# Performance work log

Hardware: AMD Instinct MI355X
Metric: run time of the kernel (lower is better)

## Reference

```python
import jax, jax.numpy as jnp
import numpy as np

B, S, D = 2, 2048, 768
H = 12
DK = D // H  # 64; dim_q = dim_k = dim_v
DFF = 3072
EPS = 1e-5


def layer_norm(x, w, b):
    mu = jnp.mean(x, axis=-1, keepdims=True)
    var = jnp.var(x, axis=-1, keepdims=True)
    return (x - mu) * jax.lax.rsqrt(var + EPS) * w + b


def setup_inputs() -> dict:
    key = jax.random.key(0)
    ks = jax.random.split(key, 12)
    s = 0.02
    return {
        "src": jax.random.normal(ks[0], (B, S, D), dtype=jnp.float32),
        # per-head projections stacked over heads: [H, D, DK]
        "Wq": jax.random.normal(ks[1], (H, D, DK), dtype=jnp.float32) * s,
        "bq": jnp.zeros((H, DK), dtype=jnp.float32),
        "Wk": jax.random.normal(ks[2], (H, D, DK), dtype=jnp.float32) * s,
        "bk": jnp.zeros((H, DK), dtype=jnp.float32),
        "Wv": jax.random.normal(ks[3], (H, D, DK), dtype=jnp.float32) * s,
        "bv": jnp.zeros((H, DK), dtype=jnp.float32),
        # output projection: [H*DK, D]
        "Wo": jax.random.normal(ks[4], (H * DK, D), dtype=jnp.float32) * s,
        "bo": jnp.zeros((D,), dtype=jnp.float32),
        "ln1_w": jnp.ones((D,), dtype=jnp.float32),
        "ln1_b": jnp.zeros((D,), dtype=jnp.float32),
        "W1": jax.random.normal(ks[5], (D, DFF), dtype=jnp.float32) * s,
        "b1": jnp.zeros((DFF,), dtype=jnp.float32),
        "W2": jax.random.normal(ks[6], (DFF, D), dtype=jnp.float32) * s,
        "b2": jnp.zeros((D,), dtype=jnp.float32),
        "ln2_w": jnp.ones((D,), dtype=jnp.float32),
        "ln2_b": jnp.zeros((D,), dtype=jnp.float32),
    }


def reference(src, Wq, bq, Wk, bk, Wv, bv, Wo, bo, ln1_w, ln1_b,
              W1, b1, W2, b2, ln2_w, ln2_b):
    # per-head q/k/v projections, batched over heads via einsum
    q = jnp.einsum('bsd,hdk->bhsk', src, Wq) + bq[None, :, None, :]
    k = jnp.einsum('bsd,hdk->bhsk', src, Wk) + bk[None, :, None, :]
    v = jnp.einsum('bsd,hdk->bhsk', src, Wv) + bv[None, :, None, :]
    scale = jnp.asarray(DK, src.dtype) ** 0.5
    scores = jnp.einsum('bhsk,bhtk->bhst', q, k) / scale  # [B,H,S,S]
    attn = jax.nn.softmax(scores, axis=-1)
    ctx = jnp.einsum('bhst,bhtk->bhsk', attn, v)
    # concat heads along feature dim (matches torch.cat over head outputs)
    ctx = ctx.transpose(0, 2, 1, 3).reshape(src.shape[0], src.shape[1], H * DK)
    attn_out = ctx @ Wo + bo
    x = layer_norm(src + attn_out, ln1_w, ln1_b)
    ff = jax.nn.relu(x @ W1 + b1) @ W2 + b2
    return layer_norm(x + ff, ln2_w, ln2_b)
```

## Files before the change

### kernel.cpp

```cpp
#include <hip/hip_runtime.h>
#include <hip/hip_bf16.h>

#define S_LEN 2048
#define DMODEL 768
#define NHEAD 12
#define DKH 64
#define DFF_K 3072
#define MROWS 4096
#define KSPLIT 2
#define KHALF (S_LEN / KSPLIT)

typedef __attribute__((ext_vector_type(8))) short bf16x8;
typedef __attribute__((ext_vector_type(8))) unsigned short us8;
typedef __attribute__((ext_vector_type(4))) float f32x4;

__device__ __forceinline__ float bfu2f(unsigned short u) {
  return __uint_as_float(((unsigned int)u) << 16);
}
__device__ __forceinline__ unsigned short f2bfu(float f) {
  __hip_bfloat16 h = __float2bfloat16(f);
  return *reinterpret_cast<unsigned short*>(&h);
}

__device__ __forceinline__ void async16(const unsigned short* g, unsigned short* l) {
  __builtin_amdgcn_global_load_lds(
      (const __attribute__((address_space(1))) unsigned int*)g,
      (__attribute__((address_space(3))) unsigned int*)l, 16, 0, 0);
}

__global__ __launch_bounds__(256) void convert_kernel(
    const float* __restrict__ in, unsigned short* __restrict__ out, int n4)
{
  const int i = blockIdx.x * 256 + threadIdx.x;
  if (i < n4) {
    float4 v = *(const float4*)(in + (size_t)i * 4);
    ushort4 o;
    o.x = f2bfu(v.x); o.y = f2bfu(v.y); o.z = f2bfu(v.z); o.w = f2bfu(v.w);
    *(ushort4*)(out + (size_t)i * 4) = o;
  }
}

__device__ __forceinline__ void transpose_conv_body(
    const float* in, unsigned short* out, int R, int Ctot, int head,
    int bx, int by, int tid)
{
  __shared__ float t[64][68];
  const int r0 = bx * 64;
  const int c0 = by * 64;
  const float* ib;
  int ld;
  if (head) { ib = in + (size_t)by * R * 64; ld = 64; }
  else      { ib = in + c0;                  ld = Ctot; }
  const int lr = tid >> 4;
  const int lc = (tid & 15) << 2;

#pragma unroll
  for (int rr = 0; rr < 4; ++rr) {
    const int row = rr * 16 + lr;
    float4 v = *(const float4*)(ib + (size_t)(r0 + row) * ld + lc);
    t[row][lc + 0] = v.x; t[row][lc + 1] = v.y;
    t[row][lc + 2] = v.z; t[row][lc + 3] = v.w;
  }
  __syncthreads();
#pragma unroll
  for (int rr = 0; rr < 4; ++rr) {
    const int oc = rr * 16 + lr;
    ushort4 o;
    o.x = f2bfu(t[lc + 0][oc]); o.y = f2bfu(t[lc + 1][oc]);
    o.z = f2bfu(t[lc + 2][oc]); o.w = f2bfu(t[lc + 3][oc]);
    *(ushort4*)(out + (size_t)(c0 + oc) * R + r0 + lc) = o;
  }
}

__global__ __launch_bounds__(256) void transpose_conv_kernel(
    const float* __restrict__ in, unsigned short* __restrict__ out,
    int R, int Ctot, int head)
{
  transpose_conv_body(in, out, R, Ctot, head, blockIdx.x, blockIdx.y, threadIdx.x);
}

__global__ __launch_bounds__(256) void transpose_conv4_kernel(
    const float* __restrict__ i0, const float* __restrict__ i1,
    const float* __restrict__ i2, const float* __restrict__ i3,
    unsigned short* __restrict__ o0, unsigned short* __restrict__ o1,
    unsigned short* __restrict__ o2, unsigned short* __restrict__ o3)
{
  const int z = blockIdx.z;
  const float* in = (z == 0) ? i0 : (z == 1) ? i1 : (z == 2) ? i2 : i3;
  unsigned short* out = (z == 0) ? o0 : (z == 1) ? o1 : (z == 2) ? o2 : o3;
  transpose_conv_body(in, out, DMODEL, DMODEL, (z < 3) ? 1 : 0,
                      blockIdx.x, blockIdx.y, threadIdx.x);
}

template<int BN>
__device__ __forceinline__ void stage_tile(
    const unsigned short* __restrict__ Ab,
    const unsigned short* __restrict__ Bb,
    unsigned short* As, unsigned short* Bs,
    int wid, int lane, int K, int kofs)
{
  const int r = lane >> 3;
  const int s = lane & 7;
#pragma unroll
  for (int p = 0; p < 4; ++p) {
    const int row = wid * 32 + p * 8 + r;
    async16(Ab + (size_t)row * K + kofs + ((s ^ (row & 7)) << 3),
            As + (size_t)(wid * 32 + p * 8) * 64);
  }
#pragma unroll
  for (int p = 0; p < BN / 32; ++p) {
    const int row = wid * (BN / 4) + p * 8 + r;
    async16(Bb + (size_t)row * K + kofs + ((s ^ (row & 7)) << 3),
            Bs + (size_t)(wid * (BN / 4) + p * 8) * 64);
  }
}

template<int BN>
__global__ __launch_bounds__(256) void mfma_gemm_kernel(
    const unsigned short* __restrict__ A,
    const unsigned short* __restrict__ BT,
    const float* __restrict__ bias,
    unsigned short* __restrict__ C,
    int K, int N, int relu, int klen, size_t out_stride)
{
  constexpr int WN = (BN == 128) ? 64 : 32;
  constexpr int NJ = WN / 16;
  __shared__ unsigned short As[2][128][64];
  __shared__ unsigned short Bs[2][BN][64];

  const int tid  = threadIdx.x;
  const int wid  = tid >> 6;
  const int lane = tid & 63;
  const int ml   = lane & 15;
  const int quad = lane >> 4;
  const int wm   = (wid & 1) * 64;
  const int wn   = (wid >> 1) * WN;
  const int row0 = blockIdx.x * 128;
  const int col0 = blockIdx.y * BN;
  const int zed  = blockIdx.z;
  const int kb0  = zed * klen;
  const int nsteps = klen >> 6;
  const int fsw = (ml & 7) << 4;

  const unsigned short* Ab = A  + (size_t)row0 * K + kb0;
  const unsigned short* Bb = BT + (size_t)col0 * K + kb0;

  f32x4 acc[4][NJ];
#pragma unroll
  for (int i = 0; i < 4; ++i)
#pragma unroll
    for (int j = 0; j < NJ; ++j)
#pragma unroll
      for (int r = 0; r < 4; ++r) acc[i][j][r] = 0.f;

  stage_tile<BN>(Ab, Bb, &As[0][0][0], &Bs[0][0][0], wid, lane, K, 0);

  for (int st = 0; st < nsteps; ++st) {
    const int cur = st & 1;
    if (st + 1 < nsteps) {
      stage_tile<BN>(Ab, Bb, &As[cur ^ 1][0][0], &Bs[cur ^ 1][0][0],
                     wid, lane, K, (st + 1) << 6);
      if constexpr (BN == 128) { asm volatile("s_waitcnt vmcnt(8)" ::: "memory"); }
      else                     { asm volatile("s_waitcnt vmcnt(6)" ::: "memory"); }
    } else {
      asm volatile("s_waitcnt vmcnt(0)" ::: "memory");
    }
    __builtin_amdgcn_s_barrier();

    const char* Ac = (const char*)&As[cur][0][0];
    const char* Bc = (const char*)&Bs[cur][0][0];
#pragma unroll
    for (int h = 0; h < 2; ++h) {
      bf16x8 af[4], bfr[NJ];
#pragma unroll
      for (int i = 0; i < 4; ++i) {
        const int ar = wm + i * 16 + ml;
        af[i] = *(const bf16x8*)(Ac + ar * 128 + (((h << 6) + (quad << 4)) ^ fsw));
      }
#pragma unroll
      for (int j = 0; j < NJ; ++j) {
        const int br = wn + j * 16 + ml;
        bfr[j] = *(const bf16x8*)(Bc + br * 128 + (((h << 6) + (quad << 4)) ^ fsw));
      }
#pragma unroll
      for (int i = 0; i < 4; ++i)
#pragma unroll
        for (int j = 0; j < NJ; ++j)
          acc[i][j] = __builtin_amdgcn_mfma_f32_16x16x32_bf16(
              af[i], bfr[j], acc[i][j], 0, 0, 0);
    }
    __builtin_amdgcn_s_barrier();
  }

  unsigned short* Cz = C + (size_t)zed * out_stride;
#pragma unroll
  for (int j = 0; j < NJ; ++j) {
    const int col = col0 + wn + j * 16 + ml;
    const float bb = (zed == 0) ? bias[col] : 0.f;
#pragma unroll
    for (int i = 0; i < 4; ++i) {
      const int r0g = row0 + wm + i * 16 + (quad << 2);
#pragma unroll
      for (int r = 0; r < 4; ++r) {
        float v = acc[i][j][r] + bb;
        if (relu) v = fmaxf(v, 0.f);
        Cz[(size_t)(r0g + r) * N + col] = f2bfu(v);
      }
    }
  }
}

__global__ __launch_bounds__(256) void qkv_gemm_kernel(
    const unsigned short* __restrict__ A,
    const unsigned short* __restrict__ W0, const unsigned short* __restrict__ W1,
    const unsigned short* __restrict__ W2,
    const float* __restrict__ bq, const float* __restrict__ bk,
    const float* __restrict__ bv,
    unsigned short* __restrict__ C0, unsigned short* __restrict__ C1,
    unsigned short* __restrict__ C2)
{
  __shared__ unsigned short As[2][128][64];
  __shared__ unsigned short Bs[2][64][64];
  const int z = blockIdx.z;
  const unsigned short* BT = (z == 0) ? W0 : (z == 1) ? W1 : W2;
  const float* bias = (z == 0) ? bq : (z == 1) ? bk : bv;
  unsigned short* C = (z == 0) ? C0 : (z == 1) ? C1 : C2;
  const int K = DMODEL, N = DMODEL;

  const int tid  = threadIdx.x;
  const int wid  = tid >> 6;
  const int lane = tid & 63;
  const int ml   = lane & 15;
  const int quad = lane >> 4;
  const int wm   = (wid & 1) * 64;
  const int wn   = (wid >> 1) * 32;
  const int row0 = blockIdx.x * 128;
  const int col0 = blockIdx.y * 64;
  const int fsw = (ml & 7) << 4;

  const unsigned short* Ab = A  + (size_t)row0 * K;
  const unsigned short* Bb = BT + (size_t)col0 * K;

  f32x4 acc[4][2];
#pragma unroll
  for (int i = 0; i < 4; ++i)
#pragma unroll
    for (int j = 0; j < 2; ++j)
#pragma unroll
      for (int r = 0; r < 4; ++r) acc[i][j][r] = 0.f;

  stage_tile<64>(Ab, Bb, &As[0][0][0], &Bs[0][0][0], wid, lane, K, 0);

  const int nsteps = K >> 6;
  for (int st = 0; st < nsteps; ++st) {
    const int cur = st & 1;
    if (st + 1 < nsteps) {
      stage_tile<64>(Ab, Bb, &As[cur ^ 1][0][0], &Bs[cur ^ 1][0][0],
                     wid, lane, K, (st + 1) << 6);
      asm volatile("s_waitcnt vmcnt(6)" ::: "memory");
    } else {
      asm volatile("s_waitcnt vmcnt(0)" ::: "memory");
    }
    __builtin_amdgcn_s_barrier();

    const char* Ac = (const char*)&As[cur][0][0];
    const char* Bc = (const char*)&Bs[cur][0][0];
#pragma unroll
    for (int h = 0; h < 2; ++h) {
      bf16x8 af[4], bfr[2];
#pragma unroll
      for (int i = 0; i < 4; ++i) {
        const int ar = wm + i * 16 + ml;
        af[i] = *(const bf16x8*)(Ac + ar * 128 + (((h << 6) + (quad << 4)) ^ fsw));
      }
#pragma unroll
      for (int j = 0; j < 2; ++j) {
        const int br = wn + j * 16 + ml;
        bfr[j] = *(const bf16x8*)(Bc + br * 128 + (((h << 6) + (quad << 4)) ^ fsw));
      }
#pragma unroll
      for (int i = 0; i < 4; ++i)
#pragma unroll
        for (int j = 0; j < 2; ++j)
          acc[i][j] = __builtin_amdgcn_mfma_f32_16x16x32_bf16(
              af[i], bfr[j], acc[i][j], 0, 0, 0);
    }
    __builtin_amdgcn_s_barrier();
  }

#pragma unroll
  for (int j = 0; j < 2; ++j) {
    const int col = col0 + wn + j * 16 + ml;
    const float bb = bias[col];
#pragma unroll
    for (int i = 0; i < 4; ++i) {
      const int r0g = row0 + wm + i * 16 + (quad << 2);
      if (z == 2) {
        const int bb_ = r0g >> 11, s = r0g & 2047;
        const int hh = col >> 6, dd = col & 63;
        ushort4 o;
        o.x = f2bfu(acc[i][j][0] + bb); o.y = f2bfu(acc[i][j][1] + bb);
        o.z = f2bfu(acc[i][j][2] + bb); o.w = f2bfu(acc[i][j][3] + bb);
        *(ushort4*)(C + ((size_t)((bb_ * NHEAD + hh) * DKH + dd)) * S_LEN + s) = o;
      } else {
#pragma unroll
        for (int r = 0; r < 4; ++r)
          C[(size_t)(r0g + r) * N + col] = f2bfu(acc[i][j][r] + bb);
      }
    }
  }
}

#define SCL2E 0.1803368822f
__global__ __launch_bounds__(256, 3) void flash_attn_mfma(
    const unsigned short* __restrict__ Q,
    const unsigned short* __restrict__ K,
    const unsigned short* __restrict__ VT,
    float* __restrict__ Opart,
    float* __restrict__ Lpart)
{
  __shared__ unsigned short Ks[64][64];
  __shared__ unsigned short Vs[64][64];
  __shared__ unsigned short QP[4][2][16][64];

  const int tid  = threadIdx.x;
  const int wid  = tid >> 6;
  const int lane = tid & 63;
  const int ml   = lane & 15;
  const int quad = lane >> 4;
  const int h    = blockIdx.x, b = blockIdx.y;
  const int q0   = (blockIdx.z >> 1) * 128;
  const int ks   = blockIdx.z & 1;
  const int kt0  = ks * KHALF;

  const size_t qkbase = ((size_t)b * S_LEN) * DMODEL + (size_t)h * DKH;
  const size_t vtbase = ((size_t)(b * NHEAD + h)) * DKH * S_LEN;

  const int sr  = tid >> 2;
  const int scb = (tid & 3) << 5;
  const int ssw = (sr & 7) << 4;
  const int fsw = (ml & 7) << 4;

  char* ksrow = (char*)&Ks[sr][0];
  char* vsrow = (char*)&Vs[sr][0];

  const int qrA = q0 + wid * 32 + ml;
  const int qrB = qrA + 16;
  const unsigned short* qpg = Q + qkbase;
  bf16x8 qfA0 = *(const bf16x8*)(qpg + (size_t)qrA * DMODEL + (quad << 3));
  bf16x8 qfA1 = *(const bf16x8*)(qpg + (size_t)qrA * DMODEL + 32 + (quad << 3));
  bf16x8 qfB0 = *(const bf16x8*)(qpg + (size_t)qrB * DMODEL + (quad << 3));
  bf16x8 qfB1 = *(const bf16x8*)(qpg + (size_t)qrB * DMODEL + 32 + (quad << 3));

  const unsigned short* pK = K + qkbase + (size_t)(kt0 + sr) * DMODEL + (scb >> 1);
  const unsigned short* pV = VT + vtbase + (size_t)sr * S_LEN + kt0 + (scb >> 1);

  float lsumA = 0.f, lsumB = 0.f;
  f32x4 oaccA[4], oaccB[4];
#pragma unroll
  for (int dt = 0; dt < 4; ++dt)
#pragma unroll
    for (int r = 0; r < 4; ++r) { oaccA[dt][r] = 0.f; oaccB[dt][r] = 0.f; }

  us8 rk0 = *(const us8*)(pK);
  us8 rk1 = *(const us8*)(pK + 8);
  us8 rv0 = *(const us8*)(pV);
  us8 rv1 = *(const us8*)(pV + 8);

  char* qpA = (char*)&QP[wid][0][ml][0];
  char* qpB = (char*)&QP[wid][1][ml][0];

  for (int kt = 0; kt < KHALF; kt += 64) {
    __syncthreads();
    *(us8*)(ksrow + ((scb +  0) ^ ssw)) = rk0;
    *(us8*)(ksrow + ((scb + 16) ^ ssw)) = rk1;
    *(us8*)(vsrow + ((scb +  0) ^ ssw)) = rv0;
    *(us8*)(vsrow + ((scb + 16) ^ ssw)) = rv1;
    __syncthreads();

    const int ktn = kt + 64;
    if (ktn < KHALF) {
      rk0 = *(const us8*)(pK + (size_t)ktn * DMODEL);
      rk1 = *(const us8*)(pK + (size_t)ktn * DMODEL + 8);
      rv0 = *(const us8*)(pV + ktn);
      rv1 = *(const us8*)(pV + ktn + 8);
    }

    f32x4 sA[4], sB[4];
#pragma unroll
    for (int mt = 0; mt < 4; ++mt)
#pragma unroll
      for (int r = 0; r < 4; ++r) { sA[mt][r] = 0.f; sB[mt][r] = 0.f; }
#pragma unroll
    for (int mt = 0; mt < 4; ++mt) {
      char* kr = (char*)&Ks[mt * 16 + ml][0];
      bf16x8 kf0 = *(const bf16x8*)(kr + (((quad << 4) +  0) ^ fsw));
      bf16x8 kf1 = *(const bf16x8*)(kr + (((quad << 4) + 64) ^ fsw));
      sA[mt] = __builtin_amdgcn_mfma_f32_16x16x32_bf16(kf0, qfA0, sA[mt], 0, 0, 0);
      sA[mt] = __builtin_amdgcn_mfma_f32_16x16x32_bf16(kf1, qfA1, sA[mt], 0, 0, 0);
      sB[mt] = __builtin_amdgcn_mfma_f32_16x16x32_bf16(kf0, qfB0, sB[mt], 0, 0, 0);
      sB[mt] = __builtin_amdgcn_mfma_f32_16x16x32_bf16(kf1, qfB1, sB[mt], 0, 0, 0);
    }

#pragma unroll
    for (int mt = 0; mt < 4; ++mt) {
      float e0 = exp2f(sA[mt][0] * SCL2E), e1 = exp2f(sA[mt][1] * SCL2E),
            e2 = exp2f(sA[mt][2] * SCL2E), e3 = exp2f(sA[mt][3] * SCL2E);
      lsumA += (e0 + e1) + (e2 + e3);
      ushort4 oA;
      oA.x = f2bfu(e0); oA.y = f2bfu(e1); oA.z = f2bfu(e2); oA.w = f2bfu(e3);
      *(ushort4*)(qpA + (((mt << 5) + (quad << 3)) ^ fsw)) = oA;
      e0 = exp2f(sB[mt][0] * SCL2E); e1 = exp2f(sB[mt][1] * SCL2E);
      e2 = exp2f(sB[mt][2] * SCL2E); e3 = exp2f(sB[mt][3] * SCL2E);
      lsumB += (e0 + e1) + (e2 + e3);
      ushort4 oB;
      oB.x = f2bfu(e0); oB.y = f2bfu(e1); oB.z = f2bfu(e2); oB.w = f2bfu(e3);
      *(ushort4*)(qpB + (((mt << 5) + (quad << 3)) ^ fsw)) = oB;
    }
    bf16x8 pfA0 = *(const bf16x8*)(qpA + (((quad << 4) +  0) ^ fsw));
    bf16x8 pfA1 = *(const bf16x8*)(qpA + (((quad << 4) + 64) ^ fsw));
    bf16x8 pfB0 = *(const bf16x8*)(qpB + (((quad << 4) +  0) ^ fsw));
    bf16x8 pfB1 = *(const bf16x8*)(qpB + (((quad << 4) + 64) ^ fsw));

#pragma unroll
    for (int dt = 0; dt < 4; ++dt) {
      char* vr = (char*)&Vs[dt * 16 + ml][0];
      bf16x8 vf0 = *(const bf16x8*)(vr + (((quad << 4) +  0) ^ fsw));
      bf16x8 vf1 = *(const bf16x8*)(vr + (((quad << 4) + 64) ^ fsw));
      oaccA[dt] = __builtin_amdgcn_mfma_f32_16x16x32_bf16(vf0, pfA0, oaccA[dt], 0, 0, 0);
      oaccA[dt] = __builtin_amdgcn_mfma_f32_16x16x32_bf16(vf1, pfA1, oaccA[dt], 0, 0, 0);
      oaccB[dt] = __builtin_amdgcn_mfma_f32_16x16x32_bf16(vf0, pfB0, oaccB[dt], 0, 0, 0);
      oaccB[dt] = __builtin_amdgcn_mfma_f32_16x16x32_bf16(vf1, pfB1, oaccB[dt], 0, 0, 0);
    }
  }

  lsumA += __shfl_xor(lsumA, 16);
  lsumA += __shfl_xor(lsumA, 32);
  lsumB += __shfl_xor(lsumB, 16);
  lsumB += __shfl_xor(lsumB, 32);
  const size_t lbase = (((size_t)(ks * 2 + b)) * NHEAD + h) * S_LEN;
  const size_t obaseA = (lbase + qrA) * DKH;
  const size_t obaseB = (lbase + qrB) * DKH;
#pragma unroll
  for (int dt = 0; dt < 4; ++dt) {
    *(f32x4*)&Opart[obaseA + dt * 16 + (quad << 2)] = oaccA[dt];
    *(f32x4*)&Opart[obaseB + dt * 16 + (quad << 2)] = oaccB[dt];
  }
  if (quad == 0) {
    Lpart[lbase + qrA] = lsumA;
    Lpart[lbase + qrB] = lsumB;
  }
}

__global__ __launch_bounds__(256) void attn_combine_kernel(
    const float* __restrict__ Op,
    const float* __restrict__ Lp,
    unsigned short* __restrict__ O)
{
  const int s = blockIdx.x & (S_LEN - 1);
  const int b = blockIdx.x >> 11;
  const int tid = threadIdx.x;
  const size_t ohalf = (size_t)2 * NHEAD * S_LEN * DKH;
  const size_t lhalf = (size_t)2 * NHEAD * S_LEN;
#pragma unroll
  for (int c = tid; c < DMODEL; c += 256) {
    const int hh = c >> 6, dd = c & 63;
    const size_t li = ((size_t)b * NHEAD + hh) * S_LEN + s;
    const size_t oi = li * DKH + dd;
    const float o = Op[oi] + Op[ohalf + oi];
    const float l = Lp[li] + Lp[lhalf + li];
    O[((size_t)b * S_LEN + s) * DMODEL + c] = f2bfu(o / l);
  }
}

__global__ __launch_bounds__(256) void add_ln_kernel(
    const void* __restrict__ X, const void* __restrict__ Y,
    const void* __restrict__ Y2,
    const float* __restrict__ w, const float* __restrict__ bvec,
    void* __restrict__ out, int xbf, int ybf, int obf)
{
  __shared__ float buf[DMODEL];
  __shared__ float rbuf[8];
  const int tid  = threadIdx.x;
  const int lane = tid & 63, wv = tid >> 6;
  const size_t base = (size_t)blockIdx.x * DMODEL;

  float s = 0.f, s2 = 0.f;
#pragma unroll
  for (int j = tid; j < DMODEL; j += 256) {
    float xv = xbf ? bfu2f(((const unsigned short*)X)[base + j])
                   : ((const float*)X)[base + j];
    float yv = ybf ? bfu2f(((const unsigned short*)Y)[base + j])
                   : ((const float*)Y)[base + j];
    float v = xv + yv;
    if (Y2) v += ybf ? bfu2f(((const unsigned short*)Y2)[base + j])
                     : ((const float*)Y2)[base + j];
    buf[j] = v; s += v; s2 += v * v;
  }
#pragma unroll
  for (int o = 32; o; o >>= 1) { s += __shfl_xor(s, o); s2 += __shfl_xor(s2, o); }
  if (lane == 0) { rbuf[wv] = s; rbuf[4 + wv] = s2; }
  __syncthreads();
  const float S  = rbuf[0] + rbuf[1] + rbuf[2] + rbuf[3];
  const float S2 = rbuf[4] + rbuf[5] + rbuf[6] + rbuf[7];
  const float mean = S * (1.f / (float)DMODEL);
  const float var  = S2 * (1.f / (float)DMODEL) - mean * mean;
  const float rstd = rsqrtf(var + 1e-5f);
#pragma unroll
  for (int j = tid; j < DMODEL; j += 256) {
    float v = (buf[j] - mean) * rstd * w[j] + bvec[j];
    if (obf) ((unsigned short*)out)[base + j] = f2bfu(v);
    else     ((float*)out)[base + j] = v;
  }
}

extern "C" void kernel_launch(void* const* d_in, const int* in_sizes, int n_in,
                              void* d_out, int out_size, void* d_ws, size_t ws_size,
                              hipStream_t stream) {
  const float* src  = (const float*)d_in[0];
  const float* Wq   = (const float*)d_in[1];
  const float* bq   = (const float*)d_in[2];
  const float* Wk   = (const float*)d_in[3];
  const float* bk   = (const float*)d_in[4];
  const float* Wv   = (const float*)d_in[5];
  const float* bv   = (const float*)d_in[6];
  const float* Wo   = (const float*)d_in[7];
  const float* bo   = (const float*)d_in[8];
  const float* ln1w = (const float*)d_in[9];
  const float* ln1b = (const float*)d_in[10];
  const float* W1   = (const float*)d_in[11];
  const float* b1   = (const float*)d_in[12];
  const float* W2   = (const float*)d_in[13];
  const float* b2   = (const float*)d_in[14];
  const float* ln2w = (const float*)d_in[15];
  const float* ln2b = (const float*)d_in[16];
  (void)ws_size; (void)in_sizes; (void)n_in; (void)out_size;

  unsigned short* p = (unsigned short*)d_ws;
  const size_t SEG = (size_t)MROWS * DMODEL;
  unsigned short* srcb = p; p += SEG;
  unsigned short* qb   = p; p += SEG;
  unsigned short* kb_  = p; p += SEG;
  unsigned short* vbT  = p; p += SEG;
  unsigned short* ctx  = p; p += SEG;
  unsigned short* ff   = p; p += (size_t)MROWS * DFF_K;
  unsigned short* wqt  = p; p += (size_t)DMODEL * DMODEL;
  unsigned short* wkt  = p; p += (size_t)DMODEL * DMODEL;
  unsigned short* wvt  = p; p += (size_t)DMODEL * DMODEL;
  unsigned short* wot  = p; p += (size_t)DMODEL * DMODEL;
  unsigned short* w1t  = p; p += (size_t)DMODEL * DFF_K;
  unsigned short* w2t  = p; p += (size_t)DMODEL * DFF_K;
  unsigned short* x1 = kb_;
  float* opart = (float*)ff;
  float* lpart = (float*)wqt;

  dim3 blk(256);

  convert_kernel<<<dim3(SEG / 1024), blk, 0, stream>>>(src, srcb, (int)(SEG / 4));
  transpose_conv4_kernel<<<dim3(12, 12, 4), blk, 0, stream>>>(
      Wq, Wk, Wv, Wo, wqt, wkt, wvt, wot);
  transpose_conv_kernel<<<dim3(12, 48), blk, 0, stream>>>(W1, w1t, DMODEL, DFF_K, 0);
  transpose_conv_kernel<<<dim3(48, 12), blk, 0, stream>>>(W2, w2t, DFF_K, DMODEL, 0);

  dim3 gqkv(MROWS / 128, DMODEL / 64, 3);
  qkv_gemm_kernel<<<gqkv, blk, 0, stream>>>(srcb, wqt, wkt, wvt, bq, bk, bv,
                                            qb, kb_, vbT);

  dim3 ga(NHEAD, 2, (S_LEN / 128) * KSPLIT);
  flash_attn_mfma<<<ga, blk, 0, stream>>>(qb, kb_, vbT, opart, lpart);
  attn_combine_kernel<<<dim3(MROWS), blk, 0, stream>>>(opart, lpart, ctx);

  dim3 gWo(MROWS / 128, DMODEL / 64, 2);
  mfma_gemm_kernel<64><<<gWo, blk, 0, stream>>>(ctx, wot, bo, qb,
                                                DMODEL, DMODEL, 0, DMODEL / 2, 2 * SEG);

  add_ln_kernel<<<dim3(MROWS), blk, 0, stream>>>(srcb, qb, vbT,
                                                 ln1w, ln1b, x1, 1, 1, 1);

  dim3 gF1(MROWS / 128, DFF_K / 128, 1);
  mfma_gemm_kernel<128><<<gF1, blk, 0, stream>>>(x1, w1t, b1, ff,
                                                 DMODEL, DFF_K, 1, DMODEL, 0);

  dim3 gW2(MROWS / 128, DMODEL / 64, 2);
  mfma_gemm_kernel<64><<<gW2, blk, 0, stream>>>(ff, w2t, b2, qb,
                                                DFF_K, DMODEL, 0, DFF_K / 2, 2 * SEG);

  add_ln_kernel<<<dim3(MROWS), blk, 0, stream>>>(x1, qb, vbT,
                                                 ln2w, ln2b, (float*)d_out, 1, 1, 0);
}
```

Before: 284.8 us.

## Fuse QKV GEMM to share A tiles; double-buffer K/V in flash attention

The QKV projection kernel now computes Q, K and V in one block, loading each A tile once and reusing it against three weight tiles. Previously each projection had its own grid z-slice and reloaded A. This cuts A traffic and launches a third as many blocks, but each block holds three times the accumulators, which raises register pressure and may lower occupancy. The flash attention kernel also double-buffers its K/V shared tiles, so the next tile is written while the current one is consumed, leaving one barrier per iteration instead of two.

Result: no change. 288.1 us (+1.2%).

```diff
diff --git a/kernel.cpp b/kernel.cpp
--- a/kernel.cpp
+++ b/kernel.cpp
@@ -210,7 +210,7 @@
   }
 }
 
-__global__ __launch_bounds__(256) void qkv_gemm_kernel(
+__global__ __launch_bounds__(256) void qkv_gemm_fused(
     const unsigned short* __restrict__ A,
     const unsigned short* __restrict__ W0, const unsigned short* __restrict__ W1,
     const unsigned short* __restrict__ W2,
@@ -220,11 +220,7 @@
     unsigned short* __restrict__ C2)
 {
   __shared__ unsigned short As[2][128][64];
-  __shared__ unsigned short Bs[2][64][64];
-  const int z = blockIdx.z;
-  const unsigned short* BT = (z == 0) ? W0 : (z == 1) ? W1 : W2;
-  const float* bias = (z == 0) ? bq : (z == 1) ? bk : bv;
-  unsigned short* C = (z == 0) ? C0 : (z == 1) ? C1 : C2;
+  __shared__ unsigned short Bs[2][3][64][64];
   const int K = DMODEL, N = DMODEL;
 
   const int tid  = threadIdx.x;
@@ -236,76 +232,111 @@
   const int wn   = (wid >> 1) * 32;
   const int row0 = blockIdx.x * 128;
   const int col0 = blockIdx.y * 64;
-  const int fsw = (ml & 7) << 4;
-
-  const unsigned short* Ab = A  + (size_t)row0 * K;
-  const unsigned short* Bb = BT + (size_t)col0 * K;
-
-  f32x4 acc[4][2];
-#pragma unroll
-  for (int i = 0; i < 4; ++i)
-#pragma unroll
-    for (int j = 0; j < 2; ++j)
-#pragma unroll
-      for (int r = 0; r < 4; ++r) acc[i][j][r] = 0.f;
-
-  stage_tile<64>(Ab, Bb, &As[0][0][0], &Bs[0][0][0], wid, lane, K, 0);
+  const int fsw  = (ml & 7) << 4;
+  const int r    = lane >> 3;
+  const int s    = lane & 7;
+
+  const unsigned short* Ab = A + (size_t)row0 * K;
+  const unsigned short* Bz0 = W0 + (size_t)col0 * K;
+  const unsigned short* Bz1 = W1 + (size_t)col0 * K;
+  const unsigned short* Bz2 = W2 + (size_t)col0 * K;
+
+  f32x4 acc[3][4][2];
+#pragma unroll
+  for (int z = 0; z < 3; ++z)
+#pragma unroll
+    for (int i = 0; i < 4; ++i)
+#pragma unroll
+      for (int j = 0; j < 2; ++j)
+#pragma unroll
+        for (int q = 0; q < 4; ++q) acc[z][i][j][q] = 0.f;
+
+#define QKV_STAGE(BUF, KOFS)                                                   \
+  {                                                                            \
+    const int ko = (KOFS);                                                     \
+    _Pragma("unroll")                                                          \
+    for (int p = 0; p < 4; ++p) {                                              \
+      const int row = wid * 32 + p * 8 + r;                                    \
+      async16(Ab + (size_t)row * K + ko + ((s ^ (row & 7)) << 3),              \
+              &As[BUF][wid * 32 + p * 8][0]);                                  \
+    }                                                                          \
+    _Pragma("unroll")                                                          \
+    for (int p = 0; p < 2; ++p) {                                              \
+      const int row = wid * 16 + p * 8 + r;                                    \
+      const size_t go = (size_t)row * K + ko + ((s ^ (row & 7)) << 3);         \
+      async16(Bz0 + go, &Bs[BUF][0][wid * 16 + p * 8][0]);                     \
+      async16(Bz1 + go, &Bs[BUF][1][wid * 16 + p * 8][0]);                     \
+      async16(Bz2 + go, &Bs[BUF][2][wid * 16 + p * 8][0]);                     \
+    }                                                                          \
+  }
+
+  QKV_STAGE(0, 0);
 
   const int nsteps = K >> 6;
   for (int st = 0; st < nsteps; ++st) {
     const int cur = st & 1;
     if (st + 1 < nsteps) {
-      stage_tile<64>(Ab, Bb, &As[cur ^ 1][0][0], &Bs[cur ^ 1][0][0],
-                     wid, lane, K, (st + 1) << 6);
-      asm volatile("s_waitcnt vmcnt(6)" ::: "memory");
+      QKV_STAGE(cur ^ 1, (st + 1) << 6);
+      asm volatile("s_waitcnt vmcnt(10)" ::: "memory");
     } else {
       asm volatile("s_waitcnt vmcnt(0)" ::: "memory");
     }
     __builtin_amdgcn_s_barrier();
 
     const char* Ac = (const char*)&As[cur][0][0];
-    const char* Bc = (const char*)&Bs[cur][0][0];
+    const char* Bc = (const char*)&Bs[cur][0][0][0];
 #pragma unroll
     for (int h = 0; h < 2; ++h) {
-      bf16x8 af[4], bfr[2];
+      bf16x8 af[4];
 #pragma unroll
       for (int i = 0; i < 4; ++i) {
         const int ar = wm + i * 16 + ml;
         af[i] = *(const bf16x8*)(Ac + ar * 128 + (((h << 6) + (quad << 4)) ^ fsw));
       }
 #pragma unroll
-      for (int j = 0; j < 2; ++j) {
-        const int br = wn + j * 16 + ml;
-        bfr[j] = *(const bf16x8*)(Bc + br * 128 + (((h << 6) + (quad << 4)) ^ fsw));
+      for (int z = 0; z < 3; ++z) {
+        bf16x8 bfr[2];
+#pragma unroll
+        for (int j = 0; j < 2; ++j) {
+          const int br = z * 64 + wn + j * 16 + ml;
+          bfr[j] = *(const bf16x8*)(Bc + br * 128 + (((h << 6) + (quad << 4)) ^ fsw));
+        }
+#pragma unroll
+        for (int i = 0; i < 4; ++i)
+#pragma unroll
+          for (int j = 0; j < 2; ++j)
+            acc[z][i][j] = __builtin_amdgcn_mfma_f32_16x16x32_bf16(
+                af[i], bfr[j], acc[z][i][j], 0, 0, 0);
       }
-#pragma unroll
-      for (int i = 0; i < 4; ++i)
-#pragma unroll
-        for (int j = 0; j < 2; ++j)
-          acc[i][j] = __builtin_amdgcn_mfma_f32_16x16x32_bf16(
-              af[i], bfr[j], acc[i][j], 0, 0, 0);
     }
     __builtin_amdgcn_s_barrier();
   }
-
-#pragma unroll
-  for (int j = 0; j < 2; ++j) {
-    const int col = col0 + wn + j * 16 + ml;
-    const float bb = bias[col];
-#pragma unroll
-    for (int i = 0; i < 4; ++i) {
-      const int r0g = row0 + wm + i * 16 + (quad << 2);
-      if (z == 2) {
-        const int bb_ = r0g >> 11, s = r0g & 2047;
-        const int hh = col >> 6, dd = col & 63;
-        ushort4 o;
-        o.x = f2bfu(acc[i][j][0] + bb); o.y = f2bfu(acc[i][j][1] + bb);
-        o.z = f2bfu(acc[i][j][2] + bb); o.w = f2bfu(acc[i][j][3] + bb);
-        *(ushort4*)(C + ((size_t)((bb_ * NHEAD + hh) * DKH + dd)) * S_LEN + s) = o;
-      } else {
-#pragma unroll
-        for (int r = 0; r < 4; ++r)
-          C[(size_t)(r0g + r) * N + col] = f2bfu(acc[i][j][r] + bb);
+#undef QKV_STAGE
+
+  const float* biases[3] = {bq, bk, bv};
+  unsigned short* Cs[3] = {C0, C1, C2};
+#pragma unroll
+  for (int z = 0; z < 3; ++z) {
+    unsigned short* C = Cs[z];
+#pragma unroll
+    for (int j = 0; j < 2; ++j) {
+      const int col = col0 + wn + j * 16 + ml;
+      const float bb = biases[z][col];
+#pragma unroll
+      for (int i = 0; i < 4; ++i) {
+        const int r0g = row0 + wm + i * 16 + (quad << 2);
+        if (z == 2) {
+          const int bb_ = r0g >> 11, ss = r0g & 2047;
+          const int hh = col >> 6, dd = col & 63;
+          ushort4 o;
+          o.x = f2bfu(acc[z][i][j][0] + bb); o.y = f2bfu(acc[z][i][j][1] + bb);
+          o.z = f2bfu(acc[z][i][j][2] + bb); o.w = f2bfu(acc[z][i][j][3] + bb);
+          *(ushort4*)(C + ((size_t)((bb_ * NHEAD + hh) * DKH + dd)) * S_LEN + ss) = o;
+        } else {
+#pragma unroll
+          for (int q = 0; q < 4; ++q)
+            C[(size_t)(r0g + q) * N + col] = f2bfu(acc[z][i][j][q] + bb);
+        }
       }
     }
   }
@@ -319,8 +350,8 @@
     float* __restrict__ Opart,
     float* __restrict__ Lpart)
 {
-  __shared__ unsigned short Ks[64][64];
-  __shared__ unsigned short Vs[64][64];
+  __shared__ unsigned short Ks[2][64][64];
+  __shared__ unsigned short Vs[2][64][64];
   __shared__ unsigned short QP[4][2][16][64];
 
   const int tid  = threadIdx.x;
@@ -341,9 +372,6 @@
   const int ssw = (sr & 7) << 4;
   const int fsw = (ml & 7) << 4;
 
-  char* ksrow = (char*)&Ks[sr][0];
-  char* vsrow = (char*)&Vs[sr][0];
-
   const int qrA = q0 + wid * 32 + ml;
   const int qrB = qrA + 16;
   const unsigned short* qpg = Q + qkbase;
@@ -362,28 +390,44 @@
 #pragma unroll
     for (int r = 0; r < 4; ++r) { oaccA[dt][r] = 0.f; oaccB[dt][r] = 0.f; }
 
+  char* qpA = (char*)&QP[wid][0][ml][0];
+  char* qpB = (char*)&QP[wid][1][ml][0];
+
   us8 rk0 = *(const us8*)(pK);
   us8 rk1 = *(const us8*)(pK + 8);
   us8 rv0 = *(const us8*)(pV);
   us8 rv1 = *(const us8*)(pV + 8);
-
-  char* qpA = (char*)&QP[wid][0][ml][0];
-  char* qpB = (char*)&QP[wid][1][ml][0];
-
-  for (int kt = 0; kt < KHALF; kt += 64) {
-    __syncthreads();
-    *(us8*)(ksrow + ((scb +  0) ^ ssw)) = rk0;
-    *(us8*)(ksrow + ((scb + 16) ^ ssw)) = rk1;
-    *(us8*)(vsrow + ((scb +  0) ^ ssw)) = rv0;
-    *(us8*)(vsrow + ((scb + 16) ^ ssw)) = rv1;
-    __syncthreads();
-
-    const int ktn = kt + 64;
-    if (ktn < KHALF) {
-      rk0 = *(const us8*)(pK + (size_t)ktn * DMODEL);
-      rk1 = *(const us8*)(pK + (size_t)ktn * DMODEL + 8);
-      rv0 = *(const us8*)(pV + ktn);
-      rv1 = *(const us8*)(pV + ktn + 8);
+  {
+    char* kw = (char*)&Ks[0][sr][0];
+    char* vw = (char*)&Vs[0][sr][0];
+    *(us8*)(kw + ((scb +  0) ^ ssw)) = rk0;
+    *(us8*)(kw + ((scb + 16) ^ ssw)) = rk1;
+    *(us8*)(vw + ((scb +  0) ^ ssw)) = rv0;
+    *(us8*)(vw + ((scb + 16) ^ ssw)) = rv1;
+  }
+  rk0 = *(const us8*)(pK + (size_t)64 * DMODEL);
+  rk1 = *(const us8*)(pK + (size_t)64 * DMODEL + 8);
+  rv0 = *(const us8*)(pV + 64);
+  rv1 = *(const us8*)(pV + 64 + 8);
+  __syncthreads();
+
+  const int NT = KHALF / 64;
+  for (int t = 0; t < NT; ++t) {
+    const int cur = t & 1;
+    if (t + 1 < NT) {
+      char* kw = (char*)&Ks[cur ^ 1][sr][0];
+      char* vw = (char*)&Vs[cur ^ 1][sr][0];
+      *(us8*)(kw + ((scb +  0) ^ ssw)) = rk0;
+      *(us8*)(kw + ((scb + 16) ^ ssw)) = rk1;
+      *(us8*)(vw + ((scb +  0) ^ ssw)) = rv0;
+      *(us8*)(vw + ((scb + 16) ^ ssw)) = rv1;
+      if (t + 2 < NT) {
+        const size_t ko = (size_t)(t + 2) * 64;
+        rk0 = *(const us8*)(pK + ko * DMODEL);
+        rk1 = *(const us8*)(pK + ko * DMODEL + 8);
+        rv0 = *(const us8*)(pV + ko);
+        rv1 = *(const us8*)(pV + ko + 8);
+      }
     }
 
     f32x4 sA[4], sB[4];
@@ -393,7 +437,7 @@
       for (int r = 0; r < 4; ++r) { sA[mt][r] = 0.f; sB[mt][r] = 0.f; }
 #pragma unroll
     for (int mt = 0; mt < 4; ++mt) {
-      char* kr = (char*)&Ks[mt * 16 + ml][0];
+      char* kr = (char*)&Ks[cur][mt * 16 + ml][0];
       bf16x8 kf0 = *(const bf16x8*)(kr + (((quad << 4) +  0) ^ fsw));
       bf16x8 kf1 = *(const bf16x8*)(kr + (((quad << 4) + 64) ^ fsw));
       sA[mt] = __builtin_amdgcn_mfma_f32_16x16x32_bf16(kf0, qfA0, sA[mt], 0, 0, 0);
@@ -424,7 +468,7 @@
 
 #pragma unroll
     for (int dt = 0; dt < 4; ++dt) {
-      char* vr = (char*)&Vs[dt * 16 + ml][0];
+      char* vr = (char*)&Vs[cur][dt * 16 + ml][0];
       bf16x8 vf0 = *(const bf16x8*)(vr + (((quad << 4) +  0) ^ fsw));
       bf16x8 vf1 = *(const bf16x8*)(vr + (((quad << 4) + 64) ^ fsw));
       oaccA[dt] = __builtin_amdgcn_mfma_f32_16x16x32_bf16(vf0, pfA0, oaccA[dt], 0, 0, 0);
@@ -432,6 +476,8 @@
       oaccB[dt] = __builtin_amdgcn_mfma_f32_16x16x32_bf16(vf0, pfB0, oaccB[dt], 0, 0, 0);
       oaccB[dt] = __builtin_amdgcn_mfma_f32_16x16x32_bf16(vf1, pfB1, oaccB[dt], 0, 0, 0);
     }
+
+    __syncthreads();
   }
 
   lsumA += __shfl_xor(lsumA, 16);
@@ -562,9 +608,9 @@
   transpose_conv_kernel<<<dim3(12, 48), blk, 0, stream>>>(W1, w1t, DMODEL, DFF_K, 0);
   transpose_conv_kernel<<<dim3(48, 12), blk, 0, stream>>>(W2, w2t, DFF_K, DMODEL, 0);
 
-  dim3 gqkv(MROWS / 128, DMODEL / 64, 3);
-  qkv_gemm_kernel<<<gqkv, blk, 0, stream>>>(srcb, wqt, wkt, wvt, bq, bk, bv,
-                                            qb, kb_, vbT);
+  dim3 gqkv(MROWS / 128, DMODEL / 64);
+  qkv_gemm_fused<<<gqkv, blk, 0, stream>>>(srcb, wqt, wkt, wvt, bq, bk, bv,
+                                           qb, kb_, vbT);
 
   dim3 ga(NHEAD, 2, (S_LEN / 128) * KSPLIT);
   flash_attn_mfma<<<ga, blk, 0, stream>>>(qb, kb_, vbT, opart, lpart);
```

## Double-buffer K/V shared tiles in flash attention and raise MFMA wave priority

Applied to the files above, without the earlier changes.

The flash attention kernel now keeps two LDS buffers each for K and V. While the current tile is being computed, the next tile is written into the other buffer, which cuts the per-iteration barrier pair down to one and lets the LDS stores overlap the MFMA work. The MFMA sections are also wrapped in s_setprio so those waves get issue priority. LDS use per block rises by 16KB, which could lower occupancy below the 3 blocks per CU requested in the launch bounds.

Measured after the change: 284.5 us. Within noise of the previous version (-0.1%).

```diff
diff --git a/kernel.cpp b/kernel.cpp
--- a/kernel.cpp
+++ b/kernel.cpp
@@ -319,8 +319,8 @@
     float* __restrict__ Opart,
     float* __restrict__ Lpart)
 {
-  __shared__ unsigned short Ks[64][64];
-  __shared__ unsigned short Vs[64][64];
+  __shared__ unsigned short Ks[2][64][64];
+  __shared__ unsigned short Vs[2][64][64];
   __shared__ unsigned short QP[4][2][16][64];
 
   const int tid  = threadIdx.x;
@@ -341,9 +341,6 @@
   const int ssw = (sr & 7) << 4;
   const int fsw = (ml & 7) << 4;
 
-  char* ksrow = (char*)&Ks[sr][0];
-  char* vsrow = (char*)&Vs[sr][0];
-
   const int qrA = q0 + wid * 32 + ml;
   const int qrB = qrA + 16;
   const unsigned short* qpg = Q + qkbase;
@@ -362,28 +359,44 @@
 #pragma unroll
     for (int r = 0; r < 4; ++r) { oaccA[dt][r] = 0.f; oaccB[dt][r] = 0.f; }
 
+  char* qpA = (char*)&QP[wid][0][ml][0];
+  char* qpB = (char*)&QP[wid][1][ml][0];
+
   us8 rk0 = *(const us8*)(pK);
   us8 rk1 = *(const us8*)(pK + 8);
   us8 rv0 = *(const us8*)(pV);
   us8 rv1 = *(const us8*)(pV + 8);
-
-  char* qpA = (char*)&QP[wid][0][ml][0];
-  char* qpB = (char*)&QP[wid][1][ml][0];
-
-  for (int kt = 0; kt < KHALF; kt += 64) {
-    __syncthreads();
-    *(us8*)(ksrow + ((scb +  0) ^ ssw)) = rk0;
-    *(us8*)(ksrow + ((scb + 16) ^ ssw)) = rk1;
-    *(us8*)(vsrow + ((scb +  0) ^ ssw)) = rv0;
-    *(us8*)(vsrow + ((scb + 16) ^ ssw)) = rv1;
-    __syncthreads();
-
-    const int ktn = kt + 64;
-    if (ktn < KHALF) {
-      rk0 = *(const us8*)(pK + (size_t)ktn * DMODEL);
-      rk1 = *(const us8*)(pK + (size_t)ktn * DMODEL + 8);
-      rv0 = *(const us8*)(pV + ktn);
-      rv1 = *(const us8*)(pV + ktn + 8);
+  {
+    char* kw = (char*)&Ks[0][sr][0];
+    char* vw = (char*)&Vs[0][sr][0];
+    *(us8*)(kw + ((scb +  0) ^ ssw)) = rk0;
+    *(us8*)(kw + ((scb + 16) ^ ssw)) = rk1;
+    *(us8*)(vw + ((scb +  0) ^ ssw)) = rv0;
+    *(us8*)(vw + ((scb + 16) ^ ssw)) = rv1;
+  }
+  rk0 = *(const us8*)(pK + (size_t)64 * DMODEL);
+  rk1 = *(const us8*)(pK + (size_t)64 * DMODEL + 8);
+  rv0 = *(const us8*)(pV + 64);
+  rv1 = *(const us8*)(pV + 64 + 8);
+  __syncthreads();
+
+  const int NT = KHALF / 64;
+  for (int t = 0; t < NT; ++t) {
+    const int cur = t & 1;
+    if (t + 1 < NT) {
+      char* kw = (char*)&Ks[cur ^ 1][sr][0];
+      char* vw = (char*)&Vs[cur ^ 1][sr][0];
+      *(us8*)(kw + ((scb +  0) ^ ssw)) = rk0;
+      *(us8*)(kw + ((scb + 16) ^ ssw)) = rk1;
+      *(us8*)(vw + ((scb +  0) ^ ssw)) = rv0;
+      *(us8*)(vw + ((scb + 16) ^ ssw)) = rv1;
+      if (t + 2 < NT) {
+        const size_t ko = (size_t)(t + 2) * 64;
+        rk0 = *(const us8*)(pK + ko * DMODEL);
+        rk1 = *(const us8*)(pK + ko * DMODEL + 8);
+        rv0 = *(const us8*)(pV + ko);
+        rv1 = *(const us8*)(pV + ko + 8);
+      }
     }
 
     f32x4 sA[4], sB[4];
@@ -391,9 +404,10 @@
     for (int mt = 0; mt < 4; ++mt)
 #pragma unroll
       for (int r = 0; r < 4; ++r) { sA[mt][r] = 0.f; sB[mt][r] = 0.f; }
+    __builtin_amdgcn_s_setprio(1);
 #pragma unroll
     for (int mt = 0; mt < 4; ++mt) {
-      char* kr = (char*)&Ks[mt * 16 + ml][0];
+      char* kr = (char*)&Ks[cur][mt * 16 + ml][0];
       bf16x8 kf0 = *(const bf16x8*)(kr + (((quad << 4) +  0) ^ fsw));
       bf16x8 kf1 = *(const bf16x8*)(kr + (((quad << 4) + 64) ^ fsw));
       sA[mt] = __builtin_amdgcn_mfma_f32_16x16x32_bf16(kf0, qfA0, sA[mt], 0, 0, 0);
@@ -401,6 +415,7 @@
       sB[mt] = __builtin_amdgcn_mfma_f32_16x16x32_bf16(kf0, qfB0, sB[mt], 0, 0, 0);
       sB[mt] = __builtin_amdgcn_mfma_f32_16x16x32_bf16(kf1, qfB1, sB[mt], 0, 0, 0);
     }
+    __builtin_amdgcn_s_setprio(0);
 
 #pragma unroll
     for (int mt = 0; mt < 4; ++mt) {
@@ -422,9 +437,10 @@
     bf16x8 pfB0 = *(const bf16x8*)(qpB + (((quad << 4) +  0) ^ fsw));
     bf16x8 pfB1 = *(const bf16x8*)(qpB + (((quad << 4) + 64) ^ fsw));
 
+    __builtin_amdgcn_s_setprio(1);
 #pragma unroll
     for (int dt = 0; dt < 4; ++dt) {
-      char* vr = (char*)&Vs[dt * 16 + ml][0];
+      char* vr = (char*)&Vs[cur][dt * 16 + ml][0];
       bf16x8 vf0 = *(const bf16x8*)(vr + (((quad << 4) +  0) ^ fsw));
       bf16x8 vf1 = *(const bf16x8*)(vr + (((quad << 4) + 64) ^ fsw));
       oaccA[dt] = __builtin_amdgcn_mfma_f32_16x16x32_bf16(vf0, pfA0, oaccA[dt], 0, 0, 0);
@@ -432,6 +448,9 @@
       oaccB[dt] = __builtin_amdgcn_mfma_f32_16x16x32_bf16(vf0, pfB0, oaccB[dt], 0, 0, 0);
       oaccB[dt] = __builtin_amdgcn_mfma_f32_16x16x32_bf16(vf1, pfB1, oaccB[dt], 0, 0, 0);
     }
+    __builtin_amdgcn_s_setprio(0);
+
+    __syncthreads();
   }
 
   lsumA += __shfl_xor(lsumA, 16);
```
